# Performance work log

Measured on AMD Instinct MI355X. Metric: run time of the kernel, lower is better.

The kernel has to match this reference:

```python
import jax, jax.numpy as jnp
import numpy as np

EMBED_DIM = 2048
N_HEADS = 32
N_GROUPS = 8
HEAD_SIZE = EMBED_DIM // N_HEADS  # 64
SCALE = HEAD_SIZE ** -0.5
B, S = 2, 2048


def setup_inputs() -> dict:
    key = jax.random.key(0)
    ks = jax.random.split(key, 7)
    kv_dim = N_GROUPS * HEAD_SIZE
    x = jax.random.normal(ks[0], (B, S, EMBED_DIM), dtype=jnp.float32)
    # Linear weights stored [in, out] (y = x @ W), matching torch nn.Linear math.
    Wq = jax.random.normal(ks[1], (EMBED_DIM, EMBED_DIM), dtype=jnp.float32) * (EMBED_DIM ** -0.5)
    Wk = jax.random.normal(ks[2], (EMBED_DIM, kv_dim), dtype=jnp.float32) * (EMBED_DIM ** -0.5)
    Wv = jax.random.normal(ks[3], (EMBED_DIM, kv_dim), dtype=jnp.float32) * (EMBED_DIM ** -0.5)
    Wo = jax.random.normal(ks[4], (EMBED_DIM, EMBED_DIM), dtype=jnp.float32) * (EMBED_DIM ** -0.5)
    bo = jnp.zeros((EMBED_DIM,), dtype=jnp.float32)
    # causal boolean mask [S, S], broadcast over batch and heads
    mask = jnp.tril(jnp.ones((S, S), dtype=jnp.bool_))
    return {"x": x, "Wq": Wq, "Wk": Wk, "Wv": Wv, "Wo": Wo, "bo": bo, "mask": mask}


def reference(x, Wq, Wk, Wv, Wo, bo, mask):
    B_, S_, E = x.shape
    q = (x @ Wq).reshape(B_, S_, N_HEADS, HEAD_SIZE).transpose(0, 2, 1, 3)   # [B,H,S,D]
    k = (x @ Wk).reshape(B_, S_, N_GROUPS, HEAD_SIZE).transpose(0, 2, 1, 3)  # [B,G,S,D]
    v = (x @ Wv).reshape(B_, S_, N_GROUPS, HEAD_SIZE).transpose(0, 2, 1, 3)
    # GQA: each KV head serves H//G consecutive query heads (matches torch expand+reshape)
    rep = N_HEADS // N_GROUPS
    k = jnp.repeat(k, rep, axis=1)  # [B,H,S,D]
    v = jnp.repeat(v, rep, axis=1)
    scores = SCALE * jnp.einsum("bhqd,bhkd->bhqk", q, k)          # [B,H,S,S]
    scores = jnp.where(mask, scores, -jnp.inf)
    weights = jax.nn.softmax(scores, axis=-1)                      # dropout in eval mode (identity)
    attn = jnp.einsum("bhqk,bhkd->bhqd", weights, v)               # [B,H,S,D]
    attn = attn.transpose(0, 2, 1, 3).reshape(B_, S_, E)
    return attn @ Wo + bo
```

## Files before the change

### kernel.cpp

```cpp
#include <hip/hip_runtime.h>
#include <hip/hip_fp16.h>

#define E_DIM 2048
#define S_LEN 2048
#define NH 32
#define HD 64
#define KV_DIM 512
#define QKV_N 3072
#define M_ROWS 4096
#define QK_SCALE 0.18033688011112042f

typedef __bf16 bf16x8 __attribute__((ext_vector_type(8)));
typedef float f32x4 __attribute__((ext_vector_type(4)));

__device__ __forceinline__ void async_lds16(const __bf16* g, __bf16* l) {
    __builtin_amdgcn_global_load_lds(
        (const __attribute__((address_space(1))) void*)g,
        (__attribute__((address_space(3))) void*)l, 16, 0, 0);
}

#define BAR() asm volatile("s_barrier" ::: "memory")

__global__ void k_convert(const float* __restrict__ x, __bf16* __restrict__ xb, int n) {
    int i = (blockIdx.x * blockDim.x + threadIdx.x) * 4;
    if (i < n) {
        float4 v = *(const float4*)(x + i);
        xb[i + 0] = (__bf16)v.x;
        xb[i + 1] = (__bf16)v.y;
        xb[i + 2] = (__bf16)v.z;
        xb[i + 3] = (__bf16)v.w;
    }
}

__global__ void k_transpose_all(const float* __restrict__ Wq, const float* __restrict__ Wk,
                                const float* __restrict__ Wv, const float* __restrict__ Wo,
                                __bf16* __restrict__ WtAll, __bf16* __restrict__ WoT) {
    const int which = blockIdx.z;
    const float* W;
    __bf16* dst;
    int N;
    float scale = 1.f;
    if (which == 0)      { W = Wq; dst = WtAll;                                    N = E_DIM;  scale = QK_SCALE; }
    else if (which == 1) { W = Wk; dst = WtAll + (size_t)E_DIM * E_DIM;            N = KV_DIM; }
    else if (which == 2) { W = Wv; dst = WtAll + (size_t)(E_DIM + KV_DIM) * E_DIM; N = KV_DIM; }
    else                 { W = Wo; dst = WoT;                                      N = E_DIM;  }
    const int n0 = blockIdx.x * 32;
    if (n0 >= N) return;
    const int k0 = blockIdx.y * 32;
    __shared__ float tile[32][33];
    int tx = threadIdx.x, ty = threadIdx.y;
#pragma unroll
    for (int j = 0; j < 4; ++j)
        tile[ty + j * 8][tx] = W[(size_t)(k0 + ty + j * 8) * N + n0 + tx];
    __syncthreads();
#pragma unroll
    for (int j = 0; j < 4; ++j)
        dst[(size_t)(n0 + ty + j * 8) * E_DIM + k0 + tx] = (__bf16)(tile[tx][ty + j * 8] * scale);
}

#define STG(g, l, bb, hh, kt) do {                                                              \
    async_lds16((g) + (size_t)((hh) * 128) * K + (size_t)(kt) * 64,                             \
                (l) + (bb) * 16384 + (hh) * 8192);                                              \
    async_lds16((g) + (size_t)((hh) * 128 + 64) * K + (size_t)(kt) * 64,                        \
                (l) + (bb) * 16384 + (hh) * 8192 + 4096);                                       \
} while (0)

#define LDA_(p, mq) do {                                                                        \
    _Pragma("unroll") for (int i_ = 0; i_ < 4; ++i_) {                                          \
        const char* rp_ = pAs + (p) * 32768 + ((mq) * 128 + rA + i_ * 16) * 128;                \
        a[i_][0] = *(const bf16x8*)(rp_ + swzk0);                                               \
        a[i_][1] = *(const bf16x8*)(rp_ + swzk1);                                               \
    }                                                                                           \
} while (0)

#define LDB_(p, nq, b) do {                                                                     \
    _Pragma("unroll") for (int j_ = 0; j_ < 2; ++j_) {                                          \
        const char* rp_ = pBs + (p) * 32768 + ((nq) * 128 + rB + j_ * 16) * 128;                \
        b[j_][0] = *(const bf16x8*)(rp_ + swzk0);                                               \
        b[j_][1] = *(const bf16x8*)(rp_ + swzk1);                                               \
    }                                                                                           \
} while (0)

#define MM(mq, nq, b) do {                                                                      \
    __builtin_amdgcn_s_setprio(1);                                                              \
    _Pragma("unroll") for (int i_ = 0; i_ < 4; ++i_)                                            \
    _Pragma("unroll") for (int j_ = 0; j_ < 2; ++j_) {                                          \
        acc[mq][nq][i_][j_] = __builtin_amdgcn_mfma_f32_16x16x32_bf16(                          \
            a[i_][0], b[j_][0], acc[mq][nq][i_][j_], 0, 0, 0);                                  \
        acc[mq][nq][i_][j_] = __builtin_amdgcn_mfma_f32_16x16x32_bf16(                          \
            a[i_][1], b[j_][1], acc[mq][nq][i_][j_], 0, 0, 0);                                  \
    }                                                                                           \
    __builtin_amdgcn_s_setprio(0);                                                              \
} while (0)

#define GROUP(p, kt, S1, S2, WAITSTMT) do {                                                     \
    LDA_(p, 0);                                                                                 \
    LDB_(p, 0, b0);                                                                             \
    if (S1) STG(gA, lA, (p) ^ 1, 1, (kt) + 1);                                                  \
    BAR(); MM(0, 0, b0); BAR();                                                                 \
    LDB_(p, 1, b1);                                                                             \
    if (S2) STG(gA, lA, (p), 0, (kt) + 2);                                                      \
    BAR(); MM(0, 1, b1); BAR();                                                                 \
    LDA_(p, 1);                                                                                 \
    if (S2) STG(gB, lB, (p), 0, (kt) + 2);                                                      \
    BAR(); MM(1, 1, b1); BAR();                                                                 \
    if (S2) STG(gB, lB, (p), 1, (kt) + 2);                                                      \
    WAITSTMT;                                                                                   \
    BAR(); MM(1, 0, b0); BAR();                                                                 \
} while (0)

__global__ __launch_bounds__(512, 2)
void k_gemm8(const __bf16* __restrict__ A, const __bf16* __restrict__ Bt,
             __bf16* __restrict__ C, int M, int N, int K) {
    __shared__ __attribute__((aligned(16))) __bf16 As[2][16384];
    __shared__ __attribute__((aligned(16))) __bf16 Bs[2][16384];
    const int T = K >> 6;
    const int nbx = N >> 8;
    const int bid = blockIdx.x;
    const int swz = (bid & 7) * ((int)gridDim.x >> 3) + (bid >> 3);
    const int m0 = (swz / nbx) << 8;
    const int n0 = (swz % nbx) << 8;

    const int t = threadIdx.x;
    const int lane = t & 63, w = t >> 6;
    const int quad = lane >> 4, l16 = lane & 15;
    const int wr = w >> 2, wc = w & 3;

    const int rbase = w * 8 + (lane >> 3);
    const int cswz = ((lane & 7) ^ (lane >> 3)) * 8;
    const __bf16* gA = A + (size_t)(m0 + rbase) * K + cswz;
    const __bf16* gB = Bt + (size_t)(n0 + rbase) * K + cswz;
    __bf16* lA = &As[0][0] + w * 512;
    __bf16* lB = &Bs[0][0] + w * 512;

    const int swzk0 = ((0 + quad) ^ (l16 & 7)) * 16;
    const int swzk1 = ((4 + quad) ^ (l16 & 7)) * 16;
    const int rA = wr * 64 + l16;
    const int rB = wc * 32 + l16;
    const char* pAs = (const char*)&As[0][0];
    const char* pBs = (const char*)&Bs[0][0];

    f32x4 acc[2][2][4][2] = {};
    bf16x8 a[4][2], b0[2][2], b1[2][2];

    STG(gA, lA, 0, 0, 0); STG(gA, lA, 0, 1, 0);
    STG(gB, lB, 0, 0, 0); STG(gB, lB, 0, 1, 0);
    STG(gA, lA, 1, 0, 1);
    STG(gB, lB, 1, 0, 1); STG(gB, lB, 1, 1, 1);
    asm volatile("s_waitcnt vmcnt(6)" ::: "memory");
    BAR();

    int p = 0;
    for (int kt = 0; kt < T - 2; ++kt) {
        GROUP(p, kt, 1, 1, asm volatile("s_waitcnt vmcnt(6)" ::: "memory"));
        p ^= 1;
    }
    GROUP(p, T - 2, 1, 0, asm volatile("s_waitcnt vmcnt(0)" ::: "memory"));
    p ^= 1;
    GROUP(p, T - 1, 0, 0, (void)0);

#pragma unroll
    for (int mq = 0; mq < 2; ++mq)
#pragma unroll
        for (int nq = 0; nq < 2; ++nq)
#pragma unroll
            for (int i = 0; i < 4; ++i)
#pragma unroll
                for (int j = 0; j < 2; ++j) {
                    const int row = m0 + mq * 128 + wr * 64 + i * 16 + quad * 4;
                    const int col = n0 + nq * 128 + wc * 32 + j * 16 + l16;
#pragma unroll
                    for (int r = 0; r < 4; ++r)
                        C[(size_t)(row + r) * N + col] = (__bf16)acc[mq][nq][i][j][r];
                }
    (void)M;
}

template <int OUT_F32>
__global__ __launch_bounds__(256, 2)
void k_gemm_bt(const __bf16* __restrict__ A, const __bf16* __restrict__ Bt,
               void* __restrict__ Cout, const float* __restrict__ bias,
               int M, int N, int K) {
    __shared__ __attribute__((aligned(16))) __bf16 As2[128 * 64];
    __shared__ __attribute__((aligned(16))) __bf16 Bs2[128 * 64];
    const int t = threadIdx.x;
    const int lane = t & 63, wave = t >> 6;
    const int quad = lane >> 4, l16 = lane & 15;
    const int wr = wave >> 1, wc = wave & 1;
    const int m0 = blockIdx.y * 128, n0 = blockIdx.x * 128;

    const int srow = t >> 2;
    const int sblk = (t & 3) ^ ((t >> 3) & 3);
    const __bf16* gA0 = A + (size_t)(m0 + srow) * K + sblk * 8;
    const __bf16* gA1 = gA0 + (size_t)64 * K;
    const __bf16* gB0 = Bt + (size_t)(n0 + srow) * K + sblk * 8;
    const __bf16* gB1 = gB0 + (size_t)64 * K;

    f32x4 acc[4][4] = {};

    for (int k0 = 0; k0 < K; k0 += 64) {
#pragma unroll
        for (int ks = 0; ks < 2; ++ks) {
            async_lds16(gA0 + k0 + ks * 32, As2 + ks * 4096 + wave * 512);
            async_lds16(gA1 + k0 + ks * 32, As2 + ks * 4096 + 2048 + wave * 512);
            async_lds16(gB0 + k0 + ks * 32, Bs2 + ks * 4096 + wave * 512);
            async_lds16(gB1 + k0 + ks * 32, Bs2 + ks * 4096 + 2048 + wave * 512);
        }
        __syncthreads();
#pragma unroll
        for (int ks = 0; ks < 2; ++ks) {
            bf16x8 af[4], bfr[4];
#pragma unroll
            for (int i = 0; i < 4; ++i) {
                const int row = wr * 64 + i * 16 + l16;
                af[i] = *(const bf16x8*)((const char*)As2 + ks * 8192 + row * 64 +
                                         ((quad ^ ((row >> 1) & 3)) * 16));
            }
#pragma unroll
            for (int j = 0; j < 4; ++j) {
                const int row = wc * 64 + j * 16 + l16;
                bfr[j] = *(const bf16x8*)((const char*)Bs2 + ks * 8192 + row * 64 +
                                          ((quad ^ ((row >> 1) & 3)) * 16));
            }
#pragma unroll
            for (int i = 0; i < 4; ++i)
#pragma unroll
                for (int j = 0; j < 4; ++j)
                    acc[i][j] = __builtin_amdgcn_mfma_f32_16x16x32_bf16(af[i], bfr[j], acc[i][j], 0, 0, 0);
        }
        __syncthreads();
    }

#pragma unroll
    for (int i = 0; i < 4; ++i)
#pragma unroll
        for (int j = 0; j < 4; ++j) {
            const int row = m0 + wr * 64 + i * 16 + quad * 4;
            const int col = n0 + wc * 64 + j * 16 + l16;
#pragma unroll
            for (int r = 0; r < 4; ++r) {
                float v = acc[i][j][r];
                if (OUT_F32) ((float*)Cout)[(size_t)(row + r) * N + col] = v + bias[col];
                else ((__bf16*)Cout)[(size_t)(row + r) * N + col] = (__bf16)v;
            }
        }
}

__global__ __launch_bounds__(256, 3)
void k_attn(const __bf16* __restrict__ qkv, __half* __restrict__ partO,
            float* __restrict__ partL) {
    const int xr = (int)(gridDim.x - 1 - blockIdx.x);
    int qi, c;
    if (xr < 8)       { qi = xr;                  c = 0; }
    else if (xr < 24) { qi = 8 + ((xr - 8) >> 1); c = (xr - 8) & 1; }
    else if (xr < 48) { qi = 16 + (xr - 24) / 3;  c = (xr - 24) % 3; }
    else              { qi = 24 + ((xr - 48) >> 2); c = (xr - 48) & 3; }
    const int q0 = qi * 64;
    const int k_lo = c * 512;
    const int k_hi = min(k_lo + 512, q0 + 64);

    const int gp = blockIdx.y;
    const int g = gp >> 1;
    const int h0 = g * 4 + (gp & 1) * 2;
    const int b = blockIdx.z;
    const int t = threadIdx.x;
    const int lane = t & 63, wave = t >> 6;
    const int quad = lane >> 4, l16 = lane & 15;

    __shared__ __attribute__((aligned(16))) __bf16 Kls[128 * 64];
    __shared__ __attribute__((aligned(16))) __bf16 vT[64][136];
    __shared__ __attribute__((aligned(16))) __bf16 pT[4][2][1024];

    const __bf16* base = qkv + (size_t)b * S_LEN * QKV_N;
    const int qrow = q0 + wave * 16 + l16;

    bf16x8 qf[2][2];
#pragma unroll
    for (int h = 0; h < 2; ++h)
#pragma unroll
        for (int s = 0; s < 2; ++s)
            qf[h][s] = *(const bf16x8*)(base + (size_t)qrow * QKV_N + (h0 + h) * HD + s * 32 + quad * 8);

    f32x4 o[2][4] = {};
    float l_st[2] = {0.f, 0.f};

    const int vkey = lane * 2, vdg = wave * 16;
    const __bf16* vsrc = base + (E_DIM + KV_DIM) + g * HD + vdg;
    const __bf16* ksrc = base + E_DIM + g * HD;

    const int klocal = lane >> 3;
    const int kdblk = (lane & 7) ^ (klocal & 7);
    const __bf16* gk_base = ksrc + (size_t)(wave * 32 + klocal) * QKV_N + kdblk * 8;
    __bf16* lk_base = Kls + wave * 2048;

    auto qk = [&](int m, f32x4* sA, f32x4* sB) {
        __builtin_amdgcn_s_setprio(1);
#pragma unroll
        for (int kt = 0; kt < 4; ++kt) {
            const int kr = m * 64 + kt * 16 + l16;
            const char* kb_ = (const char*)Kls + kr * 128;
            bf16x8 kf0 = *(const bf16x8*)(kb_ + ((quad ^ (kr & 7)) * 16));
            bf16x8 kf1 = *(const bf16x8*)(kb_ + (((4 + quad) ^ (kr & 7)) * 16));
            f32x4 z = {};
            z = __builtin_amdgcn_mfma_f32_16x16x32_bf16(kf0, qf[0][0], z, 0, 0, 0);
            sA[kt] = __builtin_amdgcn_mfma_f32_16x16x32_bf16(kf1, qf[0][1], z, 0, 0, 0);
            f32x4 ww = {};
            ww = __builtin_amdgcn_mfma_f32_16x16x32_bf16(kf0, qf[1][0], ww, 0, 0, 0);
            sB[kt] = __builtin_amdgcn_mfma_f32_16x16x32_bf16(kf1, qf[1][1], ww, 0, 0, 0);
        }
        __builtin_amdgcn_s_setprio(0);
    };

    auto softmax_p = [&](int kb, int h, f32x4* sc) {
        const bool diag = (kb == q0);
        char* prow = (char*)&pT[wave][h][0] + l16 * 128;
        float lsum = 0.f;
#pragma unroll
        for (int kt = 0; kt < 4; ++kt) {
            f32x4 pv_;
#pragma unroll
            for (int r = 0; r < 4; ++r) pv_[r] = exp2f(sc[kt][r]);
            if (diag) {
                const int kbase = kb + kt * 16 + quad * 4;
#pragma unroll
                for (int r = 0; r < 4; ++r)
                    if (kbase + r > qrow) pv_[r] = 0.f;
            }
#pragma unroll
            for (int r = 0; r < 4; ++r) lsum += pv_[r];
            __bf16 pb[4];
#pragma unroll
            for (int r = 0; r < 4; ++r) pb[r] = (__bf16)pv_[r];
            *(uint2*)(prow + ((2 * kt + (quad >> 1)) ^ (l16 & 7)) * 16 + (quad & 1) * 8) =
                *(const uint2*)pb;
        }
        l_st[h] += lsum;
    };

    auto pv = [&](int m) {
        bf16x8 vf[4][2];
        const int koff = m * 64;
#pragma unroll
        for (int cc = 0; cc < 4; ++cc)
#pragma unroll
            for (int kh = 0; kh < 2; ++kh)
                vf[cc][kh] = *(const bf16x8*)&vT[cc * 16 + l16][koff + kh * 32 + quad * 8];
        __builtin_amdgcn_s_setprio(1);
#pragma unroll
        for (int h = 0; h < 2; ++h) {
            const char* prow = (const char*)&pT[wave][h][0] + l16 * 128;
            bf16x8 pf0 = *(const bf16x8*)(prow + ((0 + quad) ^ (l16 & 7)) * 16);
            bf16x8 pf1 = *(const bf16x8*)(prow + ((4 + quad) ^ (l16 & 7)) * 16);
#pragma unroll
            for (int cc = 0; cc < 4; ++cc) {
                o[h][cc] = __builtin_amdgcn_mfma_f32_16x16x32_bf16(vf[cc][0], pf0, o[h][cc], 0, 0, 0);
                o[h][cc] = __builtin_amdgcn_mfma_f32_16x16x32_bf16(vf[cc][1], pf1, o[h][cc], 0, 0, 0);
            }
        }
        __builtin_amdgcn_s_setprio(0);
    };

    for (int kv0 = k_lo; kv0 < k_hi; kv0 += 128) {
#pragma unroll
        for (int i = 0; i < 4; ++i)
            async_lds16(gk_base + (size_t)(kv0 + i * 8) * QKV_N, lk_base + i * 512);

        const __bf16* vp = vsrc + (size_t)(kv0 + vkey) * QKV_N;
        uint4 va0 = *(const uint4*)(vp);
        uint4 va1 = *(const uint4*)(vp + 8);
        uint4 vb0 = *(const uint4*)(vp + QKV_N);
        uint4 vb1 = *(const uint4*)(vp + QKV_N + 8);

        {
            const unsigned short* a0 = (const unsigned short*)&va0;
            const unsigned short* a1 = (const unsigned short*)&va1;
            const unsigned short* b0_ = (const unsigned short*)&vb0;
            const unsigned short* b1_ = (const unsigned short*)&vb1;
#pragma unroll
            for (int j = 0; j < 8; ++j) {
                *(uint32_t*)&vT[vdg + j][vkey] = (uint32_t)a0[j] | ((uint32_t)b0_[j] << 16);
                *(uint32_t*)&vT[vdg + 8 + j][vkey] = (uint32_t)a1[j] | ((uint32_t)b1_[j] << 16);
            }
        }
        __syncthreads();

        f32x4 scA[4], scB[4];
        qk(0, scA, scB);
        softmax_p(kv0, 0, scA);
        softmax_p(kv0, 1, scB);
        pv(0);

        const int kb1 = kv0 + 64;
        if (kb1 < k_hi) {
            qk(1, scA, scB);
            softmax_p(kb1, 0, scA);
            softmax_p(kb1, 1, scB);
            pv(1);
        }
        __syncthreads();
    }

    const size_t blk = ((size_t)b * 16 + gp) * 80 + xr;
    const size_t pb = blk * (2 * 64 * 64);
#pragma unroll
    for (int h = 0; h < 2; ++h) {
        float lt = l_st[h];
        lt += __shfl_xor(lt, 16);
        lt += __shfl_xor(lt, 32);
        const float inv = 1.f / lt;
        __half* prow = partO + pb + (size_t)(h * 64 + wave * 16 + l16) * 64 + quad * 4;
#pragma unroll
        for (int dt = 0; dt < 4; ++dt) {
            __half ob[4];
#pragma unroll
            for (int r = 0; r < 4; ++r) ob[r] = __float2half(o[h][dt][r] * inv);
            *(uint2*)(prow + dt * 16) = *(const uint2*)ob;
        }
        if (quad == 0)
            partL[blk * 128 + h * 64 + wave * 16 + l16] = lt;
    }
}

__global__ __launch_bounds__(256, 4)
void k_combine(const __half* __restrict__ partO, const float* __restrict__ partL,
               __bf16* __restrict__ attnb) {
    const int qi = blockIdx.x, gp = blockIdx.y, b = blockIdx.z;
    const int nc = (qi >> 3) + 1;
    int x0;
    if (qi < 8) x0 = qi;
    else if (qi < 16) x0 = 8 + (qi - 8) * 2;
    else if (qi < 24) x0 = 24 + (qi - 16) * 3;
    else x0 = 48 + (qi - 24) * 4;

    const int t = threadIdx.x;
    const int row = t >> 1, half = t & 1;
    const int h = row >> 6, q = row & 63;
    const int d0 = half * 32;
    const size_t gbase = ((size_t)b * 16 + gp) * 80;

    float W = 0.f;
    float acc[32];
#pragma unroll
    for (int i = 0; i < 32; ++i) acc[i] = 0.f;
    for (int cc = 0; cc < nc; ++cc) {
        const float a = partL[(gbase + x0 + cc) * 128 + h * 64 + q];
        W += a;
        const __half* src = partO + (gbase + x0 + cc) * (2 * 64 * 64) + (size_t)(h * 64 + q) * 64 + d0;
#pragma unroll
        for (int i = 0; i < 32; i += 8) {
            uint4 u = *(const uint4*)(src + i);
            const __half* hs = (const __half*)&u;
#pragma unroll
            for (int j = 0; j < 8; ++j) acc[i + j] += a * __half2float(hs[j]);
        }
    }
    const float inv = 1.f / W;
    const int h_abs = (gp >> 1) * 4 + (gp & 1) * 2 + h;
    __bf16* dst = attnb + ((size_t)b * S_LEN + qi * 64 + q) * E_DIM + h_abs * 64 + d0;
#pragma unroll
    for (int i = 0; i < 32; i += 8) {
        __bf16 ob[8];
#pragma unroll
        for (int j = 0; j < 8; ++j) ob[j] = (__bf16)(acc[i + j] * inv);
        *(uint4*)(dst + i) = *(const uint4*)ob;
    }
}

extern "C" void kernel_launch(void* const* d_in, const int* in_sizes, int n_in,
                              void* d_out, int out_size, void* d_ws, size_t ws_size,
                              hipStream_t stream) {
    const float* x  = (const float*)d_in[0];
    const float* Wq = (const float*)d_in[1];
    const float* Wk = (const float*)d_in[2];
    const float* Wv = (const float*)d_in[3];
    const float* Wo = (const float*)d_in[4];
    const float* bo = (const float*)d_in[5];

    __bf16* xb    = (__bf16*)d_ws;
    __bf16* WtAll = xb + (size_t)M_ROWS * E_DIM;
    __bf16* WoT   = WtAll + (size_t)QKV_N * E_DIM;
    __bf16* qkv   = WoT + (size_t)E_DIM * E_DIM;
    __bf16* attnb = qkv + (size_t)M_ROWS * QKV_N;
    __half* partO = (__half*)(attnb + (size_t)M_ROWS * E_DIM);
    float* partL  = (float*)(partO + (size_t)2560 * 2 * 64 * 64);

    k_convert<<<(M_ROWS * E_DIM / 4 + 255) / 256, 256, 0, stream>>>(x, xb, M_ROWS * E_DIM);
    k_transpose_all<<<dim3(64, 64, 4), dim3(32, 8), 0, stream>>>(Wq, Wk, Wv, Wo, WtAll, WoT);

    k_gemm8<<<dim3((M_ROWS / 256) * (QKV_N / 256)), 512, 0, stream>>>(
        xb, WtAll, qkv, M_ROWS, QKV_N, E_DIM);

    k_attn<<<dim3(80, 16, 2), 256, 0, stream>>>(qkv, partO, partL);
    k_combine<<<dim3(32, 16, 2), 256, 0, stream>>>(partO, partL, attnb);

    k_gemm_bt<1><<<dim3(E_DIM / 128, M_ROWS / 128), 256, 0, stream>>>(
        attnb, WoT, d_out, bo, M_ROWS, E_DIM, E_DIM);
}
```

Before: 321.9 us.

## Shrink attention P staging buffer and raise occupancy to four blocks

The softmax-then-PV step now runs in 32-key halves per head, so each wave reuses one small 16x32 P tile in LDS instead of holding a 16x64 tile for both heads. This cuts the P buffer from 16 KB to 4 KB per block, and the launch bound rises from 3 to 4 blocks per CU so more blocks can overlap. In exchange there are more, smaller LDS round trips and shorter MFMA chains per head. The tighter launch bound also caps VGPRs per thread, which risks spills.

```diff
diff --git a/kernel.cpp b/kernel.cpp
--- a/kernel.cpp
+++ b/kernel.cpp
@@ -246,7 +246,7 @@
         }
 }
 
-__global__ __launch_bounds__(256, 3)
+__global__ __launch_bounds__(256, 4)
 void k_attn(const __bf16* __restrict__ qkv, __half* __restrict__ partO,
             float* __restrict__ partL) {
     const int xr = (int)(gridDim.x - 1 - blockIdx.x);
@@ -269,7 +269,7 @@
 
     __shared__ __attribute__((aligned(16))) __bf16 Kls[128 * 64];
     __shared__ __attribute__((aligned(16))) __bf16 vT[64][136];
-    __shared__ __attribute__((aligned(16))) __bf16 pT[4][2][1024];
+    __shared__ __attribute__((aligned(16))) __bf16 pT[4][512];
 
     const __bf16* base = qkv + (size_t)b * S_LEN * QKV_N;
     const int qrow = q0 + wave * 16 + l16;
@@ -292,6 +292,9 @@
     const int kdblk = (lane & 7) ^ (klocal & 7);
     const __bf16* gk_base = ksrc + (size_t)(wave * 32 + klocal) * QKV_N + kdblk * 8;
     __bf16* lk_base = Kls + wave * 2048;
+
+    const int pswz = (l16 >> 1) & 3;
+    char* prow = (char*)&pT[wave][0] + l16 * 64;
 
     auto qk = [&](int m, f32x4* sA, f32x4* sB) {
         __builtin_amdgcn_s_setprio(1);
@@ -311,12 +314,12 @@
         __builtin_amdgcn_s_setprio(0);
     };
 
-    auto softmax_p = [&](int kb, int h, f32x4* sc) {
+    auto smxh = [&](int kb, int half, int h, f32x4* sc) {
         const bool diag = (kb == q0);
-        char* prow = (char*)&pT[wave][h][0] + l16 * 128;
         float lsum = 0.f;
 #pragma unroll
-        for (int kt = 0; kt < 4; ++kt) {
+        for (int u = 0; u < 2; ++u) {
+            const int kt = 2 * half + u;
             f32x4 pv_;
 #pragma unroll
             for (int r = 0; r < 4; ++r) pv_[r] = exp2f(sc[kt][r]);
@@ -331,33 +334,34 @@
             __bf16 pb[4];
 #pragma unroll
             for (int r = 0; r < 4; ++r) pb[r] = (__bf16)pv_[r];
-            *(uint2*)(prow + ((2 * kt + (quad >> 1)) ^ (l16 & 7)) * 16 + (quad & 1) * 8) =
-                *(const uint2*)pb;
+            const int bi = (2 * u + (quad >> 1)) ^ pswz;
+            *(uint2*)(prow + bi * 16 + (quad & 1) * 8) = *(const uint2*)pb;
         }
         l_st[h] += lsum;
     };
 
-    auto pv = [&](int m) {
-        bf16x8 vf[4][2];
-        const int koff = m * 64;
+    auto pvh = [&](int h, const bf16x8* vf) {
+        bf16x8 pf = *(const bf16x8*)(prow + ((quad ^ pswz) * 16));
+        __builtin_amdgcn_s_setprio(1);
 #pragma unroll
         for (int cc = 0; cc < 4; ++cc)
-#pragma unroll
-            for (int kh = 0; kh < 2; ++kh)
-                vf[cc][kh] = *(const bf16x8*)&vT[cc * 16 + l16][koff + kh * 32 + quad * 8];
-        __builtin_amdgcn_s_setprio(1);
-#pragma unroll
-        for (int h = 0; h < 2; ++h) {
-            const char* prow = (const char*)&pT[wave][h][0] + l16 * 128;
-            bf16x8 pf0 = *(const bf16x8*)(prow + ((0 + quad) ^ (l16 & 7)) * 16);
-            bf16x8 pf1 = *(const bf16x8*)(prow + ((4 + quad) ^ (l16 & 7)) * 16);
-#pragma unroll
-            for (int cc = 0; cc < 4; ++cc) {
-                o[h][cc] = __builtin_amdgcn_mfma_f32_16x16x32_bf16(vf[cc][0], pf0, o[h][cc], 0, 0, 0);
-                o[h][cc] = __builtin_amdgcn_mfma_f32_16x16x32_bf16(vf[cc][1], pf1, o[h][cc], 0, 0, 0);
-            }
-        }
+            o[h][cc] = __builtin_amdgcn_mfma_f32_16x16x32_bf16(vf[cc], pf, o[h][cc], 0, 0, 0);
         __builtin_amdgcn_s_setprio(0);
+    };
+
+    auto process = [&](int kb, int m, f32x4* sA, f32x4* sB) {
+#pragma unroll
+        for (int half = 0; half < 2; ++half) {
+            bf16x8 vf[4];
+            const int koff = m * 64 + half * 32;
+#pragma unroll
+            for (int cc = 0; cc < 4; ++cc)
+                vf[cc] = *(const bf16x8*)&vT[cc * 16 + l16][koff + quad * 8];
+            smxh(kb, half, 0, sA);
+            pvh(0, vf);
+            smxh(kb, half, 1, sB);
+            pvh(1, vf);
+        }
     };
 
     for (int kv0 = k_lo; kv0 < k_hi; kv0 += 128) {
@@ -386,16 +390,12 @@
 
         f32x4 scA[4], scB[4];
         qk(0, scA, scB);
-        softmax_p(kv0, 0, scA);
-        softmax_p(kv0, 1, scB);
-        pv(0);
+        process(kv0, 0, scA, scB);
 
         const int kb1 = kv0 + 64;
         if (kb1 < k_hi) {
             qk(1, scA, scB);
-            softmax_p(kb1, 0, scA);
-            softmax_p(kb1, 1, scB);
-            pv(1);
+            process(kb1, 1, scA, scB);
         }
         __syncthreads();
     }
@@ -408,13 +408,13 @@
         lt += __shfl_xor(lt, 16);
         lt += __shfl_xor(lt, 32);
         const float inv = 1.f / lt;
-        __half* prow = partO + pb + (size_t)(h * 64 + wave * 16 + l16) * 64 + quad * 4;
+        __half* prowO = partO + pb + (size_t)(h * 64 + wave * 16 + l16) * 64 + quad * 4;
 #pragma unroll
         for (int dt = 0; dt < 4; ++dt) {
             __half ob[4];
 #pragma unroll
             for (int r = 0; r < 4; ++r) ob[r] = __float2half(o[h][dt][r] * inv);
-            *(uint2*)(prow + dt * 16) = *(const uint2*)ob;
+            *(uint2*)(prowO + dt * 16) = *(const uint2*)ob;
         }
         if (quad == 0)
             partL[blk * 128 + h * 64 + wave * 16 + l16] = lt;
```

After: 321.8 us. Within noise of the previous version (-0.0%).

## Replace output-projection GEMM with 8-wave double-buffered pipelined 128x256 kernel

Applied to the files above, without the earlier changes.

Replaces the simple 128x128 single-buffered output-projection GEMM with an 8-wave, 128x256-tile kernel. It double-buffers LDS, issues async global-to-LDS loads two k-steps ahead, interleaves fragment loads with MFMA groups under s_setprio, and swizzles block ids for L2 locality. The aim is to hide global-load latency and improve MFMA utilisation. In exchange it uses more LDS and registers per block and launches fewer blocks, which may hurt tail balance.

```diff
diff --git a/kernel.cpp b/kernel.cpp
--- a/kernel.cpp
+++ b/kernel.cpp
@@ -176,74 +176,122 @@
     (void)M;
 }
 
-template <int OUT_F32>
-__global__ __launch_bounds__(256, 2)
-void k_gemm_bt(const __bf16* __restrict__ A, const __bf16* __restrict__ Bt,
-               void* __restrict__ Cout, const float* __restrict__ bias,
-               int M, int N, int K) {
-    __shared__ __attribute__((aligned(16))) __bf16 As2[128 * 64];
-    __shared__ __attribute__((aligned(16))) __bf16 Bs2[128 * 64];
+#define STGA_O(bb, kt) do {                                                                     \
+    async_lds16(gA + (size_t)(kt) * 64,                  &As[bb][0] + w * 512);                  \
+    async_lds16(gA + (size_t)64 * K + (size_t)(kt) * 64, &As[bb][0] + 4096 + w * 512);          \
+} while (0)
+#define STGB_O(bb, kt, hh) do {                                                                 \
+    async_lds16(gB + (size_t)((hh) * 128) * K + (size_t)(kt) * 64,                              \
+                &Bs[bb][0] + (hh) * 8192 + w * 512);                                            \
+    async_lds16(gB + (size_t)((hh) * 128 + 64) * K + (size_t)(kt) * 64,                         \
+                &Bs[bb][0] + (hh) * 8192 + 4096 + w * 512);                                     \
+} while (0)
+
+#define LDA_O(p, mq) do {                                                                       \
+    _Pragma("unroll") for (int i_ = 0; i_ < 2; ++i_) {                                          \
+        const char* rp_ = pAs + (p) * 16384 + ((mq) * 32 + rA + i_ * 16) * 128;                 \
+        a[i_][0] = *(const bf16x8*)(rp_ + swzk0);                                               \
+        a[i_][1] = *(const bf16x8*)(rp_ + swzk1);                                               \
+    }                                                                                           \
+} while (0)
+
+#define LDB_O(p, nq, b) do {                                                                    \
+    _Pragma("unroll") for (int j_ = 0; j_ < 2; ++j_) {                                          \
+        const char* rp_ = pBs + (p) * 32768 + ((nq) * 128 + rB + j_ * 16) * 128;                \
+        b[j_][0] = *(const bf16x8*)(rp_ + swzk0);                                               \
+        b[j_][1] = *(const bf16x8*)(rp_ + swzk1);                                               \
+    }                                                                                           \
+} while (0)
+
+#define MM_O(mq, nq, b) do {                                                                    \
+    __builtin_amdgcn_s_setprio(1);                                                              \
+    _Pragma("unroll") for (int i_ = 0; i_ < 2; ++i_)                                            \
+    _Pragma("unroll") for (int j_ = 0; j_ < 2; ++j_) {                                          \
+        acc[mq][nq][i_][j_] = __builtin_amdgcn_mfma_f32_16x16x32_bf16(                          \
+            a[i_][0], b[j_][0], acc[mq][nq][i_][j_], 0, 0, 0);                                  \
+        acc[mq][nq][i_][j_] = __builtin_amdgcn_mfma_f32_16x16x32_bf16(                          \
+            a[i_][1], b[j_][1], acc[mq][nq][i_][j_], 0, 0, 0);                                  \
+    }                                                                                           \
+    __builtin_amdgcn_s_setprio(0);                                                              \
+} while (0)
+
+#define GROUP_O(p, kt, S1, S2, WAITSTMT) do {                                                   \
+    LDA_O(p, 0);                                                                                \
+    LDB_O(p, 0, b0);                                                                            \
+    if (S1) STGB_O((p) ^ 1, (kt) + 1, 1);                                                       \
+    BAR(); MM_O(0, 0, b0); BAR();                                                               \
+    LDB_O(p, 1, b1);                                                                            \
+    if (S2) STGB_O(p, (kt) + 2, 0);                                                             \
+    BAR(); MM_O(0, 1, b1); BAR();                                                               \
+    LDA_O(p, 1);                                                                                \
+    BAR(); MM_O(1, 1, b1); BAR();                                                               \
+    if (S2) STGA_O(p, (kt) + 2);                                                                \
+    WAITSTMT;                                                                                   \
+    BAR(); MM_O(1, 0, b0); BAR();                                                               \
+} while (0)
+
+__global__ __launch_bounds__(512, 2)
+void k_gemm8o(const __bf16* __restrict__ A, const __bf16* __restrict__ Bt,
+              float* __restrict__ C, const float* __restrict__ bias,
+              int M, int N, int K) {
+    __shared__ __attribute__((aligned(16))) __bf16 As[2][8192];
+    __shared__ __attribute__((aligned(16))) __bf16 Bs[2][16384];
+    const int T = K >> 6;
+    const int nbx = N >> 8;
+    const int bid = blockIdx.x;
+    const int swz = (bid & 7) * ((int)gridDim.x >> 3) + (bid >> 3);
+    const int m0 = (swz / nbx) << 7;
+    const int n0 = (swz % nbx) << 8;
+
     const int t = threadIdx.x;
-    const int lane = t & 63, wave = t >> 6;
+    const int lane = t & 63, w = t >> 6;
     const int quad = lane >> 4, l16 = lane & 15;
-    const int wr = wave >> 1, wc = wave & 1;
-    const int m0 = blockIdx.y * 128, n0 = blockIdx.x * 128;
-
-    const int srow = t >> 2;
-    const int sblk = (t & 3) ^ ((t >> 3) & 3);
-    const __bf16* gA0 = A + (size_t)(m0 + srow) * K + sblk * 8;
-    const __bf16* gA1 = gA0 + (size_t)64 * K;
-    const __bf16* gB0 = Bt + (size_t)(n0 + srow) * K + sblk * 8;
-    const __bf16* gB1 = gB0 + (size_t)64 * K;
-
-    f32x4 acc[4][4] = {};
-
-    for (int k0 = 0; k0 < K; k0 += 64) {
-#pragma unroll
-        for (int ks = 0; ks < 2; ++ks) {
-            async_lds16(gA0 + k0 + ks * 32, As2 + ks * 4096 + wave * 512);
-            async_lds16(gA1 + k0 + ks * 32, As2 + ks * 4096 + 2048 + wave * 512);
-            async_lds16(gB0 + k0 + ks * 32, Bs2 + ks * 4096 + wave * 512);
-            async_lds16(gB1 + k0 + ks * 32, Bs2 + ks * 4096 + 2048 + wave * 512);
-        }
-        __syncthreads();
-#pragma unroll
-        for (int ks = 0; ks < 2; ++ks) {
-            bf16x8 af[4], bfr[4];
-#pragma unroll
-            for (int i = 0; i < 4; ++i) {
-                const int row = wr * 64 + i * 16 + l16;
-                af[i] = *(const bf16x8*)((const char*)As2 + ks * 8192 + row * 64 +
-                                         ((quad ^ ((row >> 1) & 3)) * 16));
-            }
-#pragma unroll
-            for (int j = 0; j < 4; ++j) {
-                const int row = wc * 64 + j * 16 + l16;
-                bfr[j] = *(const bf16x8*)((const char*)Bs2 + ks * 8192 + row * 64 +
-                                          ((quad ^ ((row >> 1) & 3)) * 16));
-            }
-#pragma unroll
-            for (int i = 0; i < 4; ++i)
-#pragma unroll
-                for (int j = 0; j < 4; ++j)
-                    acc[i][j] = __builtin_amdgcn_mfma_f32_16x16x32_bf16(af[i], bfr[j], acc[i][j], 0, 0, 0);
-        }
-        __syncthreads();
-    }
-
-#pragma unroll
-    for (int i = 0; i < 4; ++i)
-#pragma unroll
-        for (int j = 0; j < 4; ++j) {
-            const int row = m0 + wr * 64 + i * 16 + quad * 4;
-            const int col = n0 + wc * 64 + j * 16 + l16;
-#pragma unroll
-            for (int r = 0; r < 4; ++r) {
-                float v = acc[i][j][r];
-                if (OUT_F32) ((float*)Cout)[(size_t)(row + r) * N + col] = v + bias[col];
-                else ((__bf16*)Cout)[(size_t)(row + r) * N + col] = (__bf16)v;
-            }
-        }
+    const int wr = w >> 2, wc = w & 3;
+
+    const int rbase = w * 8 + (lane >> 3);
+    const int cswz = ((lane & 7) ^ (lane >> 3)) * 8;
+    const __bf16* gA = A + (size_t)(m0 + rbase) * K + cswz;
+    const __bf16* gB = Bt + (size_t)(n0 + rbase) * K + cswz;
+
+    const int swzk0 = ((0 + quad) ^ (l16 & 7)) * 16;
+    const int swzk1 = ((4 + quad) ^ (l16 & 7)) * 16;
+    const int rA = wr * 64 + l16;
+    const int rB = wc * 32 + l16;
+    const char* pAs = (const char*)&As[0][0];
+    const char* pBs = (const char*)&Bs[0][0];
+
+    f32x4 acc[2][2][2][2] = {};
+    bf16x8 a[2][2], b0[2][2], b1[2][2];
+
+    STGA_O(0, 0); STGB_O(0, 0, 0); STGB_O(0, 0, 1);
+    STGB_O(1, 1, 0); STGA_O(1, 1);
+    asm volatile("s_waitcnt vmcnt(4)" ::: "memory");
+    BAR();
+
+    int p = 0;
+    for (int kt = 0; kt < T - 2; ++kt) {
+        GROUP_O(p, kt, 1, 1, asm volatile("s_waitcnt vmcnt(4)" ::: "memory"));
+        p ^= 1;
+    }
+    GROUP_O(p, T - 2, 1, 0, asm volatile("s_waitcnt vmcnt(0)" ::: "memory"));
+    p ^= 1;
+    GROUP_O(p, T - 1, 0, 0, (void)0);
+
+#pragma unroll
+    for (int mq = 0; mq < 2; ++mq)
+#pragma unroll
+        for (int nq = 0; nq < 2; ++nq)
+#pragma unroll
+            for (int i = 0; i < 2; ++i)
+#pragma unroll
+                for (int j = 0; j < 2; ++j) {
+                    const int row = m0 + wr * 64 + mq * 32 + i * 16 + quad * 4;
+                    const int col = n0 + nq * 128 + wc * 32 + j * 16 + l16;
+#pragma unroll
+                    for (int r = 0; r < 4; ++r)
+                        C[(size_t)(row + r) * N + col] = acc[mq][nq][i][j][r] + bias[col];
+                }
+    (void)M;
 }
 
 __global__ __launch_bounds__(256, 3)
@@ -408,13 +456,13 @@
         lt += __shfl_xor(lt, 16);
         lt += __shfl_xor(lt, 32);
         const float inv = 1.f / lt;
-        __half* prow = partO + pb + (size_t)(h * 64 + wave * 16 + l16) * 64 + quad * 4;
+        __half* prowO = partO + pb + (size_t)(h * 64 + wave * 16 + l16) * 64 + quad * 4;
 #pragma unroll
         for (int dt = 0; dt < 4; ++dt) {
             __half ob[4];
 #pragma unroll
             for (int r = 0; r < 4; ++r) ob[r] = __float2half(o[h][dt][r] * inv);
-            *(uint2*)(prow + dt * 16) = *(const uint2*)ob;
+            *(uint2*)(prowO + dt * 16) = *(const uint2*)ob;
         }
         if (quad == 0)
             partL[blk * 128 + h * 64 + wave * 16 + l16] = lt;
@@ -493,6 +541,6 @@
     k_attn<<<dim3(80, 16, 2), 256, 0, stream>>>(qkv, partO, partL);
     k_combine<<<dim3(32, 16, 2), 256, 0, stream>>>(partO, partL, attnb);
 
-    k_gemm_bt<1><<<dim3(E_DIM / 128, M_ROWS / 128), 256, 0, stream>>>(
-        attnb, WoT, d_out, bo, M_ROWS, E_DIM, E_DIM);
-}
+    k_gemm8o<<<dim3((M_ROWS / 128) * (E_DIM / 256)), 512, 0, stream>>>(
+        attnb, WoT, (float*)d_out, bo, M_ROWS, E_DIM, E_DIM);
+}
```

After: 318.3 us. About the same (-1.1%).
